# Kernel tuning notes

Measured on AMD Instinct MI355X. Metric: run time of the kernel, lower is better.

## Reference

```python
import jax, jax.numpy as jnp
import numpy as np

N = 100000
IN_DIM = 256
OUT_DIM = 256
E = 3200000
SLOPE = 0.2


def setup_inputs() -> dict:
    key = jax.random.key(0)
    ks = jax.random.split(key, 14)
    xav = lambda k, shape: jax.random.normal(k, shape, jnp.float32) * np.sqrt(2.0 / sum(shape))
    inp = {
        "H": jax.random.normal(ks[0], (N, IN_DIM), jnp.float32),
        "W0": xav(ks[1], (IN_DIM, OUT_DIM)),
        "W1": xav(ks[2], (IN_DIM, OUT_DIM)),
        "W2": xav(ks[3], (IN_DIM, OUT_DIM)),
        "a0": xav(ks[4], (2 * OUT_DIM,)),
        "a1": xav(ks[5], (2 * OUT_DIM,)),
        "a2": xav(ks[6], (2 * OUT_DIM,)),
        "bias": jnp.zeros((OUT_DIM,), jnp.float32),
    }
    for i, r in enumerate(["0", "1", "2"]):
        inp["row" + r] = jax.random.randint(ks[7 + 2 * i], (E,), 0, N, jnp.int32)
        inp["col" + r] = jax.random.randint(ks[8 + 2 * i], (E,), 0, N, jnp.int32)
    return inp


def _gat_type(H, W, a, row, col):
    # Wh: [N, out_dim]
    Wh = H @ W
    # attention logits per edge: leaky_relu(a_dst . Wh[row] + a_src . Wh[col])
    s_dst = Wh @ a[:OUT_DIM]   # [N]
    s_src = Wh @ a[OUT_DIM:]   # [N]
    e = jax.nn.leaky_relu(s_dst[row] + s_src[col], SLOPE)  # [E]
    # segment softmax over destination node (row)
    e_max = jax.ops.segment_max(e, row, num_segments=N)    # [N]
    e_shifted = jnp.exp(e - e_max[row])
    e_sum = jax.ops.segment_sum(e_shifted, row, num_segments=N)
    alpha = e_shifted / jnp.maximum(e_sum[row], 1e-12)     # [E]
    # weighted aggregation of source features into destinations
    return jax.ops.segment_sum(alpha[:, None] * Wh[col], row, num_segments=N)


def reference(H, row0, col0, row1, col1, row2, col2, W0, W1, W2, a0, a1, a2, bias):
    out = _gat_type(H, W0, a0, row0, col0)
    out = out + _gat_type(H, W1, a1, row1, col1)
    out = out + _gat_type(H, W2, a2, row2, col2)
    return out + bias
```

## Files before the change

### kernel.cpp

```cpp
#include <hip/hip_runtime.h>
#include <cstdint>
#include <cstddef>

#define DIM 256
#define SLOPE 0.2f
#define BSHIFT 8
#define SLOTS 9216
#define TILE 4096

typedef __attribute__((ext_vector_type(8))) short short8;
typedef __attribute__((ext_vector_type(4))) float f32x4;

__device__ __forceinline__ unsigned short f2bf(float f) {
  unsigned u = __float_as_uint(f);
  u += 0x7fffu + ((u >> 16) & 1u);
  return (unsigned short)(u >> 16);
}
__device__ __forceinline__ float bf2f(unsigned short h) {
  return __uint_as_float(((unsigned)h) << 16);
}

__global__ void wtrans_kernel(const float* __restrict__ W0, const float* __restrict__ W1,
                              const float* __restrict__ W2, unsigned short* __restrict__ Wt) {
  const float* W = blockIdx.y == 0 ? W0 : (blockIdx.y == 1 ? W1 : W2);
  int k = blockIdx.x, n = threadIdx.x;
  Wt[((size_t)blockIdx.y * DIM + n) * DIM + k] = f2bf(W[k * DIM + n]);
}

__global__ __launch_bounds__(256, 2) void gemm_scores_kernel(
    const float* __restrict__ H, const unsigned short* __restrict__ Wt,
    const float* __restrict__ a, unsigned short* __restrict__ Whb,
    float* __restrict__ s_dst, float* __restrict__ s_src, int N) {
  __shared__ unsigned short Hs[64][264];
  __shared__ unsigned short Os[4][16][264];
  const int t = threadIdx.x;
  const int r0 = blockIdx.x * 64;
#pragma unroll
  for (int i = 0; i < 16; ++i) {
    int idx = t + i * 256;
    int row = idx >> 6;
    int c4 = idx & 63;
    int r = r0 + row;
    float4 h = (r < N) ? *(const float4*)&H[(size_t)r * DIM + c4 * 4]
                       : make_float4(0.f, 0.f, 0.f, 0.f);
    unsigned lo = (unsigned)f2bf(h.x) | ((unsigned)f2bf(h.y) << 16);
    unsigned hi = (unsigned)f2bf(h.z) | ((unsigned)f2bf(h.w) << 16);
    *(uint2*)&Hs[row][c4 * 4] = make_uint2(lo, hi);
  }
  __syncthreads();
  const int wave = t >> 6, lane = t & 63;
  const int q = lane >> 4, m = lane & 15;
  const int rowbase = wave * 16;
  short8 Af[8];
#pragma unroll
  for (int k0 = 0; k0 < 8; ++k0)
    Af[k0] = *(const short8*)&Hs[rowbase + m][k0 * 32 + q * 8];
  f32x4 acc[16];
#pragma unroll
  for (int j = 0; j < 16; ++j) acc[j] = (f32x4){0.f, 0.f, 0.f, 0.f};
#pragma unroll
  for (int k0 = 0; k0 < 8; ++k0) {
#pragma unroll
    for (int j = 0; j < 16; ++j) {
      short8 Bf = *(const short8*)&Wt[(size_t)(j * 16 + m) * DIM + k0 * 32 + q * 8];
      acc[j] = __builtin_amdgcn_mfma_f32_16x16x32_bf16(Af[k0], Bf, acc[j], 0, 0, 0);
    }
  }
  float pd[4] = {0, 0, 0, 0}, ps[4] = {0, 0, 0, 0};
#pragma unroll
  for (int j = 0; j < 16; ++j) {
    int col = j * 16 + m;
    float ad = a[col], as = a[DIM + col];
#pragma unroll
    for (int reg = 0; reg < 4; ++reg) {
      float v = acc[j][reg];
      pd[reg] += v * ad;
      ps[reg] += v * as;
      Os[wave][q * 4 + reg][col] = f2bf(v);
    }
  }
#pragma unroll
  for (int off = 8; off >= 1; off >>= 1) {
#pragma unroll
    for (int reg = 0; reg < 4; ++reg) {
      pd[reg] += __shfl_down(pd[reg], off);
      ps[reg] += __shfl_down(ps[reg], off);
    }
  }
  if (m == 0) {
#pragma unroll
    for (int reg = 0; reg < 4; ++reg) {
      int r = r0 + rowbase + q * 4 + reg;
      if (r < N) {
        s_dst[r] = pd[reg];
        s_src[r] = ps[reg];
      }
    }
  }
  __syncthreads();
#pragma unroll
  for (int row = 0; row < 16; ++row) {
    int r = r0 + rowbase + row;
    if (r < N)
      *(uint2*)&Whb[(size_t)r * DIM + lane * 4] = *(const uint2*)&Os[wave][row][lane * 4];
  }
}

__global__ __launch_bounds__(256) void bin_edges_kernel(
    const int* __restrict__ r0, const int* __restrict__ r1, const int* __restrict__ r2,
    const int* __restrict__ c0, const int* __restrict__ c1, const int* __restrict__ c2,
    int* __restrict__ bcnt,
    unsigned* __restrict__ pairs,
    int E, int NB) {
  __shared__ int hist[512];
  __shared__ int curs[512];
  const int ty = blockIdx.y;
  const int* rr = ty == 0 ? r0 : (ty == 1 ? r1 : r2);
  const int* cc = ty == 0 ? c0 : (ty == 1 ? c1 : c2);
  const int t = threadIdx.x;
  const int base = blockIdx.x * TILE;
  for (int i = t; i < NB; i += 256) hist[i] = 0;
  __syncthreads();
  int rows[TILE / 256];
#pragma unroll
  for (int i = 0; i < TILE / 256; ++i) {
    int e = base + t + i * 256;
    int r = (e < E) ? rr[e] : -1;
    rows[i] = r;
    if (r >= 0) atomicAdd(&hist[r >> BSHIFT], 1);
  }
  __syncthreads();
  for (int b = t; b < NB; b += 256) {
    int h = hist[b];
    int off = h ? atomicAdd(&bcnt[ty * NB + b], h) : 0;
    curs[b] = b * SLOTS + off;
  }
  __syncthreads();
  unsigned* pt = pairs + (size_t)ty * NB * SLOTS;
#pragma unroll
  for (int i = 0; i < TILE / 256; ++i) {
    int e = base + t + i * 256;
    if (e >= E) continue;
    int r = rows[i];
    int b = r >> BSHIFT;
    int pos = atomicAdd(&curs[b], 1);
    if (pos - b * SLOTS < SLOTS)
      pt[pos] = ((unsigned)(r & 255) << 17) | (unsigned)cc[e];
  }
}

__global__ __launch_bounds__(256) void bucket_sort_kernel(
    const int* __restrict__ bcnt, unsigned* __restrict__ pairs,
    int* __restrict__ rp, int* __restrict__ deg, int N, int NB) {
  __shared__ int hist[256];
  __shared__ int excl[256];
  __shared__ int curs[256];
  __shared__ unsigned stage[SLOTS];
  const int b = blockIdx.x, ty = blockIdx.y;
  const int t = threadIdx.x;
  int cnt = bcnt[ty * NB + b];
  if (cnt > SLOTS) cnt = SLOTS;
  unsigned* pb = pairs + (size_t)ty * NB * SLOTS + (size_t)b * SLOTS;
  hist[t] = 0;
  __syncthreads();
  for (int i = t; i < cnt; i += 256) atomicAdd(&hist[pb[i] >> 17], 1);
  __syncthreads();
  int v = hist[t];
  excl[t] = v;
  __syncthreads();
  for (int off = 1; off < 256; off <<= 1) {
    int u = (t >= off) ? excl[t - off] : 0;
    __syncthreads();
    excl[t] += u;
    __syncthreads();
  }
  int ex = excl[t] - v;
  curs[t] = ex;
  int r = (b << BSHIFT) + t;
  if (r < N) {
    rp[(size_t)ty * N + r] = b * SLOTS + ex;
    deg[(size_t)ty * N + r] = v;
  }
  __syncthreads();
  for (int i = t; i < cnt; i += 256) {
    unsigned p = pb[i];
    int pos = atomicAdd(&curs[p >> 17], 1);
    stage[pos] = p;
  }
  __syncthreads();
  for (int i = t; i < cnt; i += 256) pb[i] = stage[i];
}

__global__ __launch_bounds__(256) void gat_fused_kernel(
    const int* __restrict__ rp, const int* __restrict__ deg,
    const unsigned* __restrict__ pairs,
    const float* __restrict__ s_dst, const float* __restrict__ s_src,
    const unsigned short* __restrict__ Whb,
    const float* __restrict__ bias, float* __restrict__ out, int N, int NB) {
  __shared__ uint2 ebuf[4][64];
  int n = (int)((blockIdx.x * (unsigned)blockDim.x + threadIdx.x) >> 6);
  if (n >= N) return;
  const int wid = (threadIdx.x >> 6);
  const int lane = threadIdx.x & 63;
  const size_t NDIM = (size_t)N * DIM;
  float4 total = {0.f, 0.f, 0.f, 0.f};
  for (int t = 0; t < 3; ++t) {
    int beg = rp[(size_t)t * N + n], d = deg[(size_t)t * N + n];
    if (d == 0) continue;
    int end = beg + d;
    const unsigned* pcol = pairs + (size_t)t * NB * SLOTS;
    const float* ss = s_src + (size_t)t * N;
    float sd = s_dst[(size_t)t * N + n];
    const unsigned short* wbase = Whb + (size_t)t * NDIM + lane * 4;
    float mx = -__builtin_inff();
    for (int p = beg + lane; p < end; p += 64) {
      float v = sd + ss[pcol[p] & 0x1FFFFu];
      v = v > 0.f ? v : SLOPE * v;
      mx = fmaxf(mx, v);
    }
#pragma unroll
    for (int off = 32; off >= 1; off >>= 1) mx = fmaxf(mx, __shfl_down(mx, off));
    mx = __shfl(mx, 0);
    float4 acc = {0.f, 0.f, 0.f, 0.f};
    float psum = 0.f;
    for (int base = beg; base < end; base += 64) {
      int myp = base + lane;
      int cnt = end - base;
      if (cnt > 64) cnt = 64;
      unsigned myc = 0;
      float mype = 0.f;
      if (myp < end) {
        myc = pcol[myp] & 0x1FFFFu;
        float v = sd + ss[myc];
        v = v > 0.f ? v : SLOPE * v;
        mype = __expf(v - mx);
      }
      psum += mype;
      ebuf[wid][lane] = make_uint2(myc, __float_as_uint(mype));
#pragma unroll 8
      for (int j = 0; j < cnt; ++j) {
        uint2 cp = ebuf[wid][j];
        float pe = __uint_as_float(cp.y);
        ushort4 w = *(const ushort4*)&wbase[(size_t)cp.x * DIM];
        acc.x += pe * bf2f(w.x);
        acc.y += pe * bf2f(w.y);
        acc.z += pe * bf2f(w.z);
        acc.w += pe * bf2f(w.w);
      }
    }
#pragma unroll
    for (int off = 32; off >= 1; off >>= 1) psum += __shfl_down(psum, off);
    psum = __shfl(psum, 0);
    float inv = 1.f / fmaxf(psum, 1e-12f);
    total.x += acc.x * inv;
    total.y += acc.y * inv;
    total.z += acc.z * inv;
    total.w += acc.w * inv;
  }
  float4 cur = ((const float4*)bias)[lane];
  cur.x += total.x;
  cur.y += total.y;
  cur.z += total.z;
  cur.w += total.w;
  *((float4*)(out + (size_t)n * DIM) + lane) = cur;
}

__global__ __launch_bounds__(256) void gat_node_kernel(
    const int* __restrict__ rp, const int* __restrict__ deg,
    const unsigned* __restrict__ pcol,
    const float* __restrict__ s_dst, const float* __restrict__ s_src,
    const unsigned short* __restrict__ Whb,
    const float* __restrict__ bias, float* __restrict__ out, int N, int first) {
  __shared__ uint2 ebuf[4][64];
  int n = (int)((blockIdx.x * (unsigned)blockDim.x + threadIdx.x) >> 6);
  if (n >= N) return;
  const int wid = (threadIdx.x >> 6);
  const int lane = threadIdx.x & 63;
  int beg = rp[n], d = deg[n], end = beg + d;
  if (!first && d == 0) return;
  float sd = s_dst[n];
  float mx = -__builtin_inff();
  for (int p = beg + lane; p < end; p += 64) {
    float v = sd + s_src[pcol[p] & 0x1FFFFu];
    v = v > 0.f ? v : SLOPE * v;
    mx = fmaxf(mx, v);
  }
#pragma unroll
  for (int off = 32; off >= 1; off >>= 1) mx = fmaxf(mx, __shfl_down(mx, off));
  mx = __shfl(mx, 0);
  const unsigned short* wbase = Whb + lane * 4;
  float4 acc = {0.f, 0.f, 0.f, 0.f};
  float psum = 0.f;
  for (int base = beg; base < end; base += 64) {
    int myp = base + lane;
    int cnt = end - base;
    if (cnt > 64) cnt = 64;
    unsigned myc = 0;
    float mype = 0.f;
    if (myp < end) {
      myc = pcol[myp] & 0x1FFFFu;
      float v = sd + s_src[myc];
      v = v > 0.f ? v : SLOPE * v;
      mype = __expf(v - mx);
    }
    psum += mype;
    ebuf[wid][lane] = make_uint2(myc, __float_as_uint(mype));
#pragma unroll 8
    for (int j = 0; j < cnt; ++j) {
      uint2 cp = ebuf[wid][j];
      float pe = __uint_as_float(cp.y);
      ushort4 w = *(const ushort4*)&wbase[(size_t)cp.x * DIM];
      acc.x += pe * bf2f(w.x);
      acc.y += pe * bf2f(w.y);
      acc.z += pe * bf2f(w.z);
      acc.w += pe * bf2f(w.w);
    }
  }
#pragma unroll
  for (int off = 32; off >= 1; off >>= 1) psum += __shfl_down(psum, off);
  psum = __shfl(psum, 0);
  float inv = 1.f / fmaxf(psum, 1e-12f);
  float4* o = (float4*)(out + (size_t)n * DIM) + lane;
  float4 cur = first ? ((const float4*)bias)[lane] : *o;
  cur.x += acc.x * inv;
  cur.y += acc.y * inv;
  cur.z += acc.z * inv;
  cur.w += acc.w * inv;
  *o = cur;
}

static inline size_t align256(size_t x) { return (x + 255) & ~(size_t)255; }

extern "C" void kernel_launch(void* const* d_in, const int* in_sizes, int n_in,
                              void* d_out, int out_size, void* d_ws, size_t ws_size,
                              hipStream_t stream) {
  const float* H = (const float*)d_in[0];
  const float* W[3] = {(const float*)d_in[1], (const float*)d_in[2], (const float*)d_in[3]};
  const float* a[3] = {(const float*)d_in[4], (const float*)d_in[5], (const float*)d_in[6]};
  const float* bias = (const float*)d_in[7];
  const int* row[3] = {(const int*)d_in[8], (const int*)d_in[10], (const int*)d_in[12]};
  const int* col[3] = {(const int*)d_in[9], (const int*)d_in[11], (const int*)d_in[13]};
  const int N = in_sizes[0] / DIM;
  const int E = in_sizes[8];
  const int NB = (N + 255) >> BSHIFT;
  float* out = (float*)d_out;

  char* ws = (char*)d_ws;
  size_t off = 0;
  unsigned short* Wt = (unsigned short*)(ws + off);
  off = align256(off + (size_t)3 * DIM * DIM * sizeof(unsigned short));
  float* s_dst = (float*)(ws + off);
  off = align256(off + (size_t)3 * N * sizeof(float));
  float* s_src = (float*)(ws + off);
  off = align256(off + (size_t)3 * N * sizeof(float));
  int* bcnt = (int*)(ws + off);
  off = align256(off + (size_t)3 * NB * sizeof(int));
  int* rp = (int*)(ws + off);
  off = align256(off + (size_t)3 * N * sizeof(int));
  int* deg = (int*)(ws + off);
  off = align256(off + (size_t)3 * N * sizeof(int));
  unsigned* pairs = (unsigned*)(ws + off);
  off = align256(off + (size_t)3 * NB * SLOTS * sizeof(unsigned));
  unsigned short* Whb = (unsigned short*)(ws + off);
  const size_t whb_bytes = align256((size_t)N * DIM * sizeof(unsigned short));
  const int fused = (ws_size >= off + 3 * whb_bytes) ? 1 : 0;

  wtrans_kernel<<<dim3(DIM, 3), 256, 0, stream>>>(W[0], W[1], W[2], Wt);
  hipMemsetAsync(bcnt, 0, (size_t)3 * NB * sizeof(int), stream);
  const int eb = (E + TILE - 1) / TILE;
  bin_edges_kernel<<<dim3(eb, 3), 256, 0, stream>>>(row[0], row[1], row[2], col[0], col[1],
                                                    col[2], bcnt, pairs, E, NB);
  bucket_sort_kernel<<<dim3(NB, 3), 256, 0, stream>>>(bcnt, pairs, rp, deg, N, NB);

  const int gemm_blocks = (N + 63) / 64;
  const int gat_blocks = (N * 64 + 255) / 256;
  if (fused) {
    for (int t = 0; t < 3; ++t)
      gemm_scores_kernel<<<gemm_blocks, 256, 0, stream>>>(
          H, Wt + (size_t)t * DIM * DIM, a[t],
          Whb + t * (whb_bytes / sizeof(unsigned short)),
          s_dst + (size_t)t * N, s_src + (size_t)t * N, N);
    gat_fused_kernel<<<gat_blocks, 256, 0, stream>>>(rp, deg, pairs, s_dst, s_src, Whb, bias,
                                                     out, N, NB);
  } else {
    for (int t = 0; t < 3; ++t) {
      gemm_scores_kernel<<<gemm_blocks, 256, 0, stream>>>(H, Wt + (size_t)t * DIM * DIM, a[t],
                                                          Whb, s_dst + (size_t)t * N,
                                                          s_src + (size_t)t * N, N);
      gat_node_kernel<<<gat_blocks, 256, 0, stream>>>(
          rp + (size_t)t * N, deg + (size_t)t * N, pairs + (size_t)t * NB * SLOTS,
          s_dst + (size_t)t * N, s_src + (size_t)t * N, Whb, bias, out, N, t == 0 ? 1 : 0);
    }
  }
  (void)n_in;
  (void)out_size;
  (void)ws_size;
}
```

Measured before the change: 1.533 ms.

## Split wave into two half-waves gathering two edges per step with 16-byte loads

The fused GAT kernel now has each half of a 64-lane wave handle a different edge, with each lane loading 8 bf16 values (16 bytes) instead of 4. This halves the serial edge loop count and doubles bytes per load, and the two partial sums are combined with a cross-half shuffle at the end. It also adds a single-pass fast path for nodes with at most 64 edges, which skips the separate max pass and reuses the logits. In exchange it uses more registers for the 8-wide accumulators and may read one padding ebuf slot when the edge count is odd.

```diff
diff --git a/kernel.cpp b/kernel.cpp
--- a/kernel.cpp
+++ b/kernel.cpp
@@ -9,6 +9,7 @@
 #define TILE 4096
 
 typedef __attribute__((ext_vector_type(8))) short short8;
+typedef __attribute__((ext_vector_type(8))) unsigned short ushort8;
 typedef __attribute__((ext_vector_type(4))) float f32x4;
 
 __device__ __forceinline__ unsigned short f2bf(float f) {
@@ -197,72 +198,103 @@
     const float* __restrict__ s_dst, const float* __restrict__ s_src,
     const unsigned short* __restrict__ Whb,
     const float* __restrict__ bias, float* __restrict__ out, int N, int NB) {
-  __shared__ uint2 ebuf[4][64];
+  __shared__ uint2 ebuf[4][65];
   int n = (int)((blockIdx.x * (unsigned)blockDim.x + threadIdx.x) >> 6);
   if (n >= N) return;
   const int wid = (threadIdx.x >> 6);
   const int lane = threadIdx.x & 63;
+  const int half = lane >> 5;
+  const int sub = lane & 31;
   const size_t NDIM = (size_t)N * DIM;
-  float4 total = {0.f, 0.f, 0.f, 0.f};
+  float total[8];
+#pragma unroll
+  for (int k = 0; k < 8; ++k) total[k] = 0.f;
   for (int t = 0; t < 3; ++t) {
     int beg = rp[(size_t)t * N + n], d = deg[(size_t)t * N + n];
     if (d == 0) continue;
-    int end = beg + d;
     const unsigned* pcol = pairs + (size_t)t * NB * SLOTS;
     const float* ss = s_src + (size_t)t * N;
     float sd = s_dst[(size_t)t * N + n];
-    const unsigned short* wbase = Whb + (size_t)t * NDIM + lane * 4;
-    float mx = -__builtin_inff();
-    for (int p = beg + lane; p < end; p += 64) {
-      float v = sd + ss[pcol[p] & 0x1FFFFu];
-      v = v > 0.f ? v : SLOPE * v;
-      mx = fmaxf(mx, v);
-    }
-#pragma unroll
-    for (int off = 32; off >= 1; off >>= 1) mx = fmaxf(mx, __shfl_down(mx, off));
-    mx = __shfl(mx, 0);
-    float4 acc = {0.f, 0.f, 0.f, 0.f};
+    const unsigned short* wb = Whb + (size_t)t * NDIM + sub * 8;
+    float acc[8];
+#pragma unroll
+    for (int k = 0; k < 8; ++k) acc[k] = 0.f;
     float psum = 0.f;
-    for (int base = beg; base < end; base += 64) {
-      int myp = base + lane;
-      int cnt = end - base;
-      if (cnt > 64) cnt = 64;
+    if (d <= 64) {
       unsigned myc = 0;
-      float mype = 0.f;
-      if (myp < end) {
-        myc = pcol[myp] & 0x1FFFFu;
-        float v = sd + ss[myc];
-        v = v > 0.f ? v : SLOPE * v;
-        mype = __expf(v - mx);
+      float v = -__builtin_inff();
+      if (lane < d) {
+        myc = pcol[beg + lane] & 0x1FFFFu;
+        float s = sd + ss[myc];
+        v = s > 0.f ? s : SLOPE * s;
       }
-      psum += mype;
+      float mx = v;
+#pragma unroll
+      for (int off = 32; off >= 1; off >>= 1) mx = fmaxf(mx, __shfl_down(mx, off));
+      mx = __shfl(mx, 0);
+      float mype = (lane < d) ? __expf(v - mx) : 0.f;
+      psum = mype;
       ebuf[wid][lane] = make_uint2(myc, __float_as_uint(mype));
 #pragma unroll 8
-      for (int j = 0; j < cnt; ++j) {
-        uint2 cp = ebuf[wid][j];
+      for (int j = 0; j < d; j += 2) {
+        uint2 cp = ebuf[wid][j + half];
         float pe = __uint_as_float(cp.y);
-        ushort4 w = *(const ushort4*)&wbase[(size_t)cp.x * DIM];
-        acc.x += pe * bf2f(w.x);
-        acc.y += pe * bf2f(w.y);
-        acc.z += pe * bf2f(w.z);
-        acc.w += pe * bf2f(w.w);
+        ushort8 w = *(const ushort8*)&wb[(size_t)cp.x * DIM];
+#pragma unroll
+        for (int k = 0; k < 8; ++k) acc[k] += pe * bf2f(w[k]);
+      }
+    } else {
+      int end = beg + d;
+      float mx = -__builtin_inff();
+      for (int p = beg + lane; p < end; p += 64) {
+        float s = sd + ss[pcol[p] & 0x1FFFFu];
+        s = s > 0.f ? s : SLOPE * s;
+        mx = fmaxf(mx, s);
+      }
+#pragma unroll
+      for (int off = 32; off >= 1; off >>= 1) mx = fmaxf(mx, __shfl_down(mx, off));
+      mx = __shfl(mx, 0);
+      for (int base = beg; base < end; base += 64) {
+        int myp = base + lane;
+        int cnt = end - base;
+        if (cnt > 64) cnt = 64;
+        unsigned myc = 0;
+        float mype = 0.f;
+        if (myp < end) {
+          myc = pcol[myp] & 0x1FFFFu;
+          float s = sd + ss[myc];
+          s = s > 0.f ? s : SLOPE * s;
+          mype = __expf(s - mx);
+        }
+        psum += mype;
+        ebuf[wid][lane] = make_uint2(myc, __float_as_uint(mype));
+#pragma unroll 8
+        for (int j = 0; j < cnt; j += 2) {
+          uint2 cp = ebuf[wid][j + half];
+          float pe = __uint_as_float(cp.y);
+          ushort8 w = *(const ushort8*)&wb[(size_t)cp.x * DIM];
+#pragma unroll
+          for (int k = 0; k < 8; ++k) acc[k] += pe * bf2f(w[k]);
+        }
       }
     }
 #pragma unroll
     for (int off = 32; off >= 1; off >>= 1) psum += __shfl_down(psum, off);
     psum = __shfl(psum, 0);
     float inv = 1.f / fmaxf(psum, 1e-12f);
-    total.x += acc.x * inv;
-    total.y += acc.y * inv;
-    total.z += acc.z * inv;
-    total.w += acc.w * inv;
-  }
-  float4 cur = ((const float4*)bias)[lane];
-  cur.x += total.x;
-  cur.y += total.y;
-  cur.z += total.z;
-  cur.w += total.w;
-  *((float4*)(out + (size_t)n * DIM) + lane) = cur;
+#pragma unroll
+    for (int k = 0; k < 8; ++k) total[k] += acc[k] * inv;
+  }
+#pragma unroll
+  for (int k = 0; k < 8; ++k) total[k] += __shfl_xor(total[k], 32);
+  int db = sub * 8 + half * 4;
+  float4 bv = *(const float4*)&bias[db];
+  float4 cur;
+  cur.x = bv.x + total[half * 4 + 0];
+  cur.y = bv.y + total[half * 4 + 1];
+  cur.z = bv.z + total[half * 4 + 2];
+  cur.w = bv.w + total[half * 4 + 3];
+  *(float4*)&out[(size_t)n * DIM + db] = cur;
 }
 
 __global__ __launch_bounds__(256) void gat_node_kernel(
```

Result: no change. 1.549 ms (+1.1%).
